# Optimization experiments

Hardware: AMD Instinct MI355X
Metric: run time of the kernel (lower is better)

Reference implementation:

```python
import jax, jax.numpy as jnp
import numpy as np

N = 50000

def gcn_conv(x, src, dst, W, b):
    # PyG GCNConv: h = x @ W; symmetric norm with self-loops; out = Ahat h + b
    h = x @ W  # [N, F]
    e = src.shape[0]
    deg = jax.ops.segment_sum(jnp.ones((e,), h.dtype), dst, num_segments=N) + 1.0  # +1 self-loop
    dinv = jax.lax.rsqrt(deg)  # deg >= 1 so finite
    norm = dinv[src] * dinv[dst]  # [E]
    agg = jax.ops.segment_sum(h[src] * norm[:, None], dst, num_segments=N)
    agg = agg + h * (dinv * dinv)[:, None]  # self-loop contribution
    return agg + b


def setup_inputs() -> dict:
    key = jax.random.key(0)
    ks = jax.random.split(key, 12)
    E = 400000
    x = jax.random.normal(ks[0], (N, 768), dtype=jnp.float32)
    edge_index = jax.random.randint(ks[1], (2, E), 0, N, dtype=jnp.int32)
    dims = [(768, 1536), (1536, 768), (768, 384), (384, 192), (192, 5)]
    inp = {"x": x, "edge_index": edge_index}
    for i, (fi, fo) in enumerate(dims):
        s = 1.0 / np.sqrt(fi)
        inp[f"W{i+1}"] = jax.random.uniform(ks[2 + 2 * i], (fi, fo), jnp.float32, -s, s)
        inp[f"b{i+1}"] = jnp.zeros((fo,), jnp.float32)
    return inp


def reference(x, edge_index, W1, b1, W2, b2, W3, b3, W4, b4, W5, b5):
    src, dst = edge_index[0], edge_index[1]
    h = x
    for W, b in [(W1, b1), (W2, b2), (W3, b3), (W4, b4)]:
        h = jax.nn.relu(gcn_conv(h, src, dst, W, b))
        # F.dropout with training=False is identity (eval mode)
    out = gcn_conv(h, src, dst, W5, b5)
    return (h, out)
```

## Files before the change

### kernel.cpp

```cpp
#include <hip/hip_runtime.h>
#include <stdint.h>

typedef unsigned short u16;
typedef unsigned int   u32;

#define NN 50000
#define NE 400000

typedef __bf16 bf16x8 __attribute__((ext_vector_type(8)));
typedef u16    u16x8  __attribute__((ext_vector_type(8)));
typedef float  f32x4  __attribute__((ext_vector_type(4)));

__device__ __forceinline__ float bf2f(u16 b) {
  union { u32 u; float f; } v; v.u = ((u32)b) << 16; return v.f;
}
__device__ __forceinline__ u16 f2bf(float f) {
  union { float f; u32 u; } v; v.f = f;
  u32 r = v.u + 0x7fffu + ((v.u >> 16) & 1u);
  return (u16)(r >> 16);
}


__global__ void zero_int_kernel(int* __restrict__ p, int n) {
  int i = blockIdx.x * blockDim.x + threadIdx.x;
  if (i < n) p[i] = 0;
}

__global__ void count_deg_kernel(const int* __restrict__ dst, int* __restrict__ deg, int e) {
  int i = blockIdx.x * blockDim.x + threadIdx.x;
  if (i < e) atomicAdd(&deg[dst[i]], 1);
}

__global__ void dinv_kernel(const int* __restrict__ deg, float* __restrict__ dinv, int n) {
  int i = blockIdx.x * blockDim.x + threadIdx.x;
  if (i < n) dinv[i] = rsqrtf((float)deg[i] + 1.0f);
}

__global__ __launch_bounds__(1024) void scan_kernel(const int* __restrict__ counts,
                                                    int* __restrict__ offsets, int n) {
  __shared__ int wsums[17];
  __shared__ int carry;
  int tid = threadIdx.x;
  int lane = tid & 63, wid = tid >> 6;
  if (tid == 0) carry = 0;
  __syncthreads();
  for (int base = 0; base < n; base += 1024) {
    int i = base + tid;
    int v = (i < n) ? counts[i] : 0;
    int s = v;
    #pragma unroll
    for (int off = 1; off < 64; off <<= 1) {
      int t = __shfl_up(s, off, 64);
      if (lane >= off) s += t;
    }
    if (lane == 63) wsums[wid] = s;
    __syncthreads();
    if (tid == 0) {
      int a = 0;
      #pragma unroll
      for (int w = 0; w < 16; ++w) { int t = wsums[w]; wsums[w] = a; a += t; }
      wsums[16] = a;
    }
    __syncthreads();
    if (i < n) offsets[i] = carry + wsums[wid] + s - v;
    __syncthreads();
    if (tid == 0) carry += wsums[16];
    __syncthreads();
  }
  if (tid == 0) offsets[n] = carry;
}

__global__ void csr_fill_kernel(const int* __restrict__ src, const int* __restrict__ dst,
                                const int* __restrict__ offsets, int* __restrict__ cursor,
                                const float* __restrict__ dinv,
                                int2* __restrict__ csr_pack, int e) {
  int i = blockIdx.x * blockDim.x + threadIdx.x;
  if (i < e) {
    int s = src[i], d = dst[i];
    int pos = offsets[d] + atomicAdd(&cursor[d], 1);
    float nr = dinv[s] * dinv[d];
    csr_pack[pos] = make_int2(s, __float_as_int(nr));
  }
}

__global__ void f2bf_kernel(const float* __restrict__ in, u16* __restrict__ out, int n) {
  int i = blockIdx.x * blockDim.x + threadIdx.x;
  if (i < n) out[i] = f2bf(in[i]);
}

__global__ void wt_kernel(const float* __restrict__ W, u16* __restrict__ Wt, int K, int N) {
  int i = blockIdx.x * blockDim.x + threadIdx.x;
  if (i < K * N) {
    int k = i / N;
    int n2 = i - k * N;
    Wt[n2 * K + k] = f2bf(W[i]);
  }
}


template<int G, bool HAS_BIAS, bool RELU, bool OUT_BF, bool OUT_F32>
__global__ __launch_bounds__(256) void agg8_kernel(
    const u16* __restrict__ g, const int* __restrict__ rowptr,
    const int2* __restrict__ csr_pack,
    const float* __restrict__ dinv, const float* __restrict__ bias,
    u16* __restrict__ outb, float* __restrict__ outf)
{
  constexpr int F = G * 8;
  int idx = blockIdx.x * blockDim.x + threadIdx.x;
  if (idx >= NN * G) return;
  int v = idx / G;
  int g8 = idx - v * G;
  const u16* base = g + g8 * 8;

  float acc[8];
  #pragma unroll
  for (int k = 0; k < 8; ++k) acc[k] = 0.f;

  int e0 = rowptr[v], e1 = rowptr[v + 1];
  int e = e0;
  for (; e + 3 < e1; e += 4) {
    int2 p0 = csr_pack[e];
    int2 p1 = csr_pack[e + 1];
    int2 p2 = csr_pack[e + 2];
    int2 p3 = csr_pack[e + 3];
    u16x8 r0 = *(const u16x8*)(base + (size_t)p0.x * F);
    u16x8 r1 = *(const u16x8*)(base + (size_t)p1.x * F);
    u16x8 r2 = *(const u16x8*)(base + (size_t)p2.x * F);
    u16x8 r3 = *(const u16x8*)(base + (size_t)p3.x * F);
    float n0 = __int_as_float(p0.y), n1 = __int_as_float(p1.y);
    float n2 = __int_as_float(p2.y), n3 = __int_as_float(p3.y);
    #pragma unroll
    for (int k = 0; k < 8; ++k) acc[k] += n0 * bf2f(r0[k]);
    #pragma unroll
    for (int k = 0; k < 8; ++k) acc[k] += n1 * bf2f(r1[k]);
    #pragma unroll
    for (int k = 0; k < 8; ++k) acc[k] += n2 * bf2f(r2[k]);
    #pragma unroll
    for (int k = 0; k < 8; ++k) acc[k] += n3 * bf2f(r3[k]);
  }
  for (; e < e1; ++e) {
    int2 p0 = csr_pack[e];
    u16x8 r0 = *(const u16x8*)(base + (size_t)p0.x * F);
    float n0 = __int_as_float(p0.y);
    #pragma unroll
    for (int k = 0; k < 8; ++k) acc[k] += n0 * bf2f(r0[k]);
  }

  float sv = dinv[v]; sv *= sv;
  u16x8 sr = *(const u16x8*)(base + (size_t)v * F);
  float vals[8];
  #pragma unroll
  for (int k = 0; k < 8; ++k) {
    float val = acc[k] + sv * bf2f(sr[k]);
    if (HAS_BIAS) val += bias[g8 * 8 + k];
    if (RELU) val = fmaxf(val, 0.f);
    vals[k] = val;
  }
  if (OUT_BF) {
    u16x8 ob;
    #pragma unroll
    for (int k = 0; k < 8; ++k) ob[k] = f2bf(vals[k]);
    *(u16x8*)(outb + (size_t)v * F + g8 * 8) = ob;
  }
  if (OUT_F32) {
    f32x4 o0, o1;
    #pragma unroll
    for (int k = 0; k < 4; ++k) { o0[k] = vals[k]; o1[k] = vals[4 + k]; }
    float* op = outf + (size_t)v * F + g8 * 8;
    *(f32x4*)op = o0;
    *(f32x4*)(op + 4) = o1;
  }
}

__global__ void agg_small_kernel(const u16* __restrict__ g, const int* __restrict__ rowptr,
                                 const int2* __restrict__ csr_pack,
                                 const float* __restrict__ dinv, const float* __restrict__ bias,
                                 float* __restrict__ out, int n, int F) {
  int idx = blockIdx.x * blockDim.x + threadIdx.x;
  if (idx >= n * F) return;
  int v = idx / F;
  int f = idx - v * F;
  float acc = 0.f;
  int e1 = rowptr[v + 1];
  for (int e = rowptr[v]; e < e1; ++e) {
    int2 p = csr_pack[e];
    acc += __int_as_float(p.y) * bf2f(g[p.x * F + f]);
  }
  float dv = dinv[v];
  out[idx] = acc + dv * dv * bf2f(g[v * F + f]) + bias[f];
}


#define BM 128
#define BN 128
#define BK 32

#define WAIT_VMCNT4 0x0F74
#define WAIT_VMCNT0 0x0F70

__device__ __forceinline__ void gl_lds16(const void* g, void* l) {
  __builtin_amdgcn_global_load_lds((const __attribute__((address_space(1))) void*)g,
                                   (__attribute__((address_space(3))) void*)l, 16, 0, 0);
}

template<bool BIAS_RELU>
__global__ __launch_bounds__(256, 4) void gemm_bt_kernel(
    const u16* __restrict__ A, const u16* __restrict__ Bt,
    u16* __restrict__ C, const float* __restrict__ bias,
    int M, int N, int K)
{
  __shared__ __align__(16) u16 As[2][BM * BK];
  __shared__ __align__(16) u16 Bs[2][BN * BK];
  int gm = (M + BM - 1) / BM;
  int gn = (N + BN - 1) / BN;
  int bid = blockIdx.x;
  int xcd = bid & 7;
  int t = bid >> 3;
  int trow = t / gn;
  int bn_i = t - trow * gn;
  int row = trow * 8 + xcd;
  if (row >= gm) return;
  int bm = row * BM, bn = bn_i * BN;

  int tid = threadIdx.x;
  int wave = tid >> 6, lane = tid & 63;
  int wm = wave & 1, wn = wave >> 1;

  int srow = tid >> 2;
  int sq_log = ((tid & 3) - ((tid >> 3) & 3)) & 3;
  int ar0 = min(bm + srow, M - 1);
  int ar1 = min(bm + 64 + srow, M - 1);
  int br0 = min(bn + srow, N - 1);
  int br1 = min(bn + 64 + srow, N - 1);
  const u16* ag0 = A + (size_t)ar0 * K + sq_log * 8;
  const u16* ag1 = A + (size_t)ar1 * K + sq_log * 8;
  const u16* bg0 = Bt + (size_t)br0 * K + sq_log * 8;
  const u16* bg1 = Bt + (size_t)br1 * K + sq_log * 8;
  int la0 = (wave * 16) * BK;
  int la1 = (64 + wave * 16) * BK;

  f32x4 acc[4][4];
  #pragma unroll
  for (int i = 0; i < 4; ++i)
    #pragma unroll
    for (int j = 0; j < 4; ++j)
      acc[i][j] = (f32x4){0.f, 0.f, 0.f, 0.f};

  int row16 = lane & 15, q = lane >> 4;
  int perm = (q + (row16 >> 1)) & 3;
  int ard = (wm * 64 + row16) * BK + perm * 8;
  int brd = (wn * 64 + row16) * BK + perm * 8;

  const int iters = K / BK;

  gl_lds16(ag0, &As[0][la0]);
  gl_lds16(ag1, &As[0][la1]);
  gl_lds16(bg0, &Bs[0][la0]);
  gl_lds16(bg1, &Bs[0][la1]);

  int buf = 0;
  for (int it = 0; it < iters; ++it) {
    __builtin_amdgcn_s_barrier();
    if (it + 1 < iters) {
      int kn = (it + 1) * BK;
      gl_lds16(ag0 + kn, &As[buf ^ 1][la0]);
      gl_lds16(ag1 + kn, &As[buf ^ 1][la1]);
      gl_lds16(bg0 + kn, &Bs[buf ^ 1][la0]);
      gl_lds16(bg1 + kn, &Bs[buf ^ 1][la1]);
      __builtin_amdgcn_s_waitcnt(WAIT_VMCNT4);
    } else {
      __builtin_amdgcn_s_waitcnt(WAIT_VMCNT0);
    }
    __builtin_amdgcn_s_barrier();

    bf16x8 af[4], bfr[4];
    #pragma unroll
    for (int i = 0; i < 4; ++i) af[i] = *(const bf16x8*)(&As[buf][ard + i * 16 * BK]);
    #pragma unroll
    for (int j = 0; j < 4; ++j) bfr[j] = *(const bf16x8*)(&Bs[buf][brd + j * 16 * BK]);
    #pragma unroll
    for (int i = 0; i < 4; ++i)
      #pragma unroll
      for (int j = 0; j < 4; ++j)
        acc[i][j] = __builtin_amdgcn_mfma_f32_16x16x32_bf16(af[i], bfr[j], acc[i][j], 0, 0, 0);
    buf ^= 1;
  }

  #pragma unroll
  for (int i = 0; i < 4; ++i) {
    int rbase = bm + wm * 64 + i * 16 + q * 4;
    #pragma unroll
    for (int j = 0; j < 4; ++j) {
      int col = bn + wn * 64 + j * 16 + row16;
      if (col < N) {
        float bv = BIAS_RELU ? bias[col] : 0.f;
        #pragma unroll
        for (int r = 0; r < 4; ++r) {
          int gr = rbase + r;
          if (gr < M) {
            float val = acc[i][j][r];
            if (BIAS_RELU) { val += bv; val = fmaxf(val, 0.f); }
            C[(size_t)gr * N + col] = f2bf(val);
          }
        }
      }
    }
  }
}

static inline int gemm_grid(int M, int N) {
  int gm = (M + BM - 1) / BM;
  int gn = (N + BN - 1) / BN;
  int rows_per_xcd = (gm + 7) / 8;
  return rows_per_xcd * gn * 8;
}


extern "C" void kernel_launch(void* const* d_in, const int* in_sizes, int n_in,
                              void* d_out, int out_size, void* d_ws, size_t ws_size,
                              hipStream_t stream) {
  const float* x   = (const float*)d_in[0];
  const int* ei    = (const int*)d_in[1];
  const int* src   = ei;
  const int* dst   = ei + NE;
  const float* W1  = (const float*)d_in[2];
  const float* b1  = (const float*)d_in[3];
  const float* W2  = (const float*)d_in[4];
  const float* b2  = (const float*)d_in[5];
  const float* W3  = (const float*)d_in[6];
  const float* b3  = (const float*)d_in[7];
  const float* W4  = (const float*)d_in[8];
  const float* b4  = (const float*)d_in[9];
  const float* W5  = (const float*)d_in[10];
  const float* b5  = (const float*)d_in[11];
  float* out_h = (float*)d_out;
  float* out_o = (float*)d_out + (size_t)NN * 192;

  char* p = (char*)d_ws;
  auto alloc = [&](size_t bytes) { char* r = p; p += (bytes + 255) & ~(size_t)255; return r; };
  int*   deg      = (int*)alloc((size_t)NN * 4);
  int*   cursor   = (int*)alloc((size_t)NN * 4);
  float* dinv     = (float*)alloc((size_t)NN * 4);
  int*   offs     = (int*)alloc((size_t)(NN + 1) * 4);
  int2*  csr_pack = (int2*)alloc((size_t)NE * 8);
  u16* W1t = (u16*)alloc((size_t)768 * 1536 * 2);
  u16* W2t = (u16*)alloc((size_t)1536 * 768 * 2);
  u16* W3t = (u16*)alloc((size_t)768 * 384 * 2);
  u16* W4t = (u16*)alloc((size_t)384 * 192 * 2);
  u16* W5t = (u16*)alloc((size_t)192 * 5 * 2);
  u16* B0 = (u16*)alloc((size_t)NN * 768 * 2);
  u16* B1 = (u16*)alloc((size_t)NN * 768 * 2);
  u16* B2 = (u16*)alloc((size_t)NN * 1536 * 2);

  u16* xb  = B0;
  u16* a0  = B1;
  u16* h1  = B2;
  u16* g2  = B0;
  u16* h2  = B1;
  u16* g3  = B0;
  u16* h3  = B2;
  u16* g4  = B0;
  u16* h4b = B1;
  u16* g5  = B0;

  const int M = NN;

  zero_int_kernel<<<(NN + 255) / 256, 256, 0, stream>>>(deg, NN);
  zero_int_kernel<<<(NN + 255) / 256, 256, 0, stream>>>(cursor, NN);
  count_deg_kernel<<<(NE + 255) / 256, 256, 0, stream>>>(dst, deg, NE);
  dinv_kernel<<<(NN + 255) / 256, 256, 0, stream>>>(deg, dinv, NN);
  scan_kernel<<<1, 1024, 0, stream>>>(deg, offs, NN);
  csr_fill_kernel<<<(NE + 255) / 256, 256, 0, stream>>>(src, dst, offs, cursor, dinv,
                                                        csr_pack, NE);
  f2bf_kernel<<<((NN * 768) + 255) / 256, 256, 0, stream>>>(x, xb, NN * 768);
  wt_kernel<<<((768 * 1536) + 255) / 256, 256, 0, stream>>>(W1, W1t, 768, 1536);
  wt_kernel<<<((1536 * 768) + 255) / 256, 256, 0, stream>>>(W2, W2t, 1536, 768);
  wt_kernel<<<((768 * 384) + 255) / 256, 256, 0, stream>>>(W3, W3t, 768, 384);
  wt_kernel<<<((384 * 192) + 255) / 256, 256, 0, stream>>>(W4, W4t, 384, 192);
  wt_kernel<<<((192 * 5) + 255) / 256, 256, 0, stream>>>(W5, W5t, 192, 5);

  dim3 blk(256);

  agg8_kernel<96, false, false, true, false><<<(NN * 96 + 255) / 256, blk, 0, stream>>>(
      xb, offs, csr_pack, dinv, nullptr, a0, nullptr);
  gemm_bt_kernel<true><<<gemm_grid(M, 1536), blk, 0, stream>>>(
      a0, W1t, h1, b1, M, 1536, 768);

  gemm_bt_kernel<false><<<gemm_grid(M, 768), blk, 0, stream>>>(
      h1, W2t, g2, nullptr, M, 768, 1536);
  agg8_kernel<96, true, true, true, false><<<(NN * 96 + 255) / 256, blk, 0, stream>>>(
      g2, offs, csr_pack, dinv, b2, h2, nullptr);

  gemm_bt_kernel<false><<<gemm_grid(M, 384), blk, 0, stream>>>(
      h2, W3t, g3, nullptr, M, 384, 768);
  agg8_kernel<48, true, true, true, false><<<(NN * 48 + 255) / 256, blk, 0, stream>>>(
      g3, offs, csr_pack, dinv, b3, h3, nullptr);

  gemm_bt_kernel<false><<<gemm_grid(M, 192), blk, 0, stream>>>(
      h3, W4t, g4, nullptr, M, 192, 384);
  agg8_kernel<24, true, true, true, true><<<(NN * 24 + 255) / 256, blk, 0, stream>>>(
      g4, offs, csr_pack, dinv, b4, h4b, out_h);

  gemm_bt_kernel<false><<<gemm_grid(M, 5), blk, 0, stream>>>(
      h4b, W5t, g5, nullptr, M, 5, 192);
  agg_small_kernel<<<((NN * 5) + 255) / 256, 256, 0, stream>>>(
      g5, offs, csr_pack, dinv, b5, out_o, NN, 5);
}
```

Measured before the change: 1.093 ms.

## Add 256x256-tile 8-wave GEMM kernel for the two largest layers

```diff
diff --git a/kernel.cpp b/kernel.cpp
--- a/kernel.cpp
+++ b/kernel.cpp
@@ -190,18 +190,175 @@
   out[idx] = acc + dv * dv * bf2f(g[v * F + f]) + bias[f];
 }
 
+#define WAIT_VMCNT4 0x0F74
+#define WAIT_VMCNT0 0x0F70
+
+__device__ __forceinline__ void gl_lds16(const void* g, void* l) {
+  __builtin_amdgcn_global_load_lds((const __attribute__((address_space(1))) void*)g,
+                                   (__attribute__((address_space(3))) void*)l, 16, 0, 0);
+}
+
+
+template<bool BIAS_RELU>
+__global__ __launch_bounds__(512, 2) void gemm256_kernel(
+    const u16* __restrict__ A, const u16* __restrict__ Bt,
+    u16* __restrict__ C, const float* __restrict__ bias,
+    int M, int N, int K)
+{
+  __shared__ __align__(16) u16 sA[2][2][256 * 32];
+  __shared__ __align__(16) u16 sB[2][2][256 * 32];
+
+  int gm = (M + 255) >> 8;
+  int gn = (N + 255) >> 8;
+  int bid = blockIdx.x;
+  int xcd = bid & 7;
+  int t = bid >> 3;
+  int trow = t / gn;
+  int bn_i = t - trow * gn;
+  int rowt = trow * 8 + xcd;
+  if (rowt >= gm) return;
+  int bm = rowt << 8, bn = bn_i << 8;
+
+  int tid = threadIdx.x;
+  int wid = tid >> 6, lane = tid & 63;
+  int wm = wid >> 2, wn = wid & 3;
+  int row16 = lane & 15, q = lane >> 4;
+
+  int sr = tid >> 2, sc = tid & 3;
+  int ar0 = min(bm + sr, M - 1);
+  int ar1 = min(bm + 128 + sr, M - 1);
+  int br0 = min(bn + sr, N - 1);
+  int br1 = min(bn + 128 + sr, N - 1);
+  const u16* Ag0 = A + (size_t)ar0 * K + sc * 8;
+  const u16* Ag1 = A + (size_t)ar1 * K + sc * 8;
+  const u16* Bg0 = Bt + (size_t)br0 * K + sc * 8;
+  const u16* Bg1 = Bt + (size_t)br1 * K + sc * 8;
+
+  f32x4 acc[8][4];
+  #pragma unroll
+  for (int m = 0; m < 8; ++m)
+    #pragma unroll
+    for (int n = 0; n < 4; ++n)
+      acc[m][n] = (f32x4){0.f, 0.f, 0.f, 0.f};
+
+  auto stageA = [&](int nb, int h, int ko) {
+    gl_lds16(Ag0 + ko, &sA[nb][h][tid * 8]);
+    gl_lds16(Ag1 + ko, &sA[nb][h][4096 + tid * 8]);
+  };
+  auto stageB = [&](int nb, int h, int ko) {
+    gl_lds16(Bg0 + ko, &sB[nb][h][tid * 8]);
+    gl_lds16(Bg1 + ko, &sB[nb][h][4096 + tid * 8]);
+  };
+
+  stageA(0, 0, 0);
+  stageB(0, 0, 0);
+  stageA(0, 1, 32);
+  stageB(0, 1, 32);
+  __builtin_amdgcn_s_waitcnt(WAIT_VMCNT4);
+  __builtin_amdgcn_s_barrier();
+
+  const int KT = K >> 6;
+  int arow = (wm * 128 + row16) * 32 + q * 8;
+  int brow = (wn * 64 + row16) * 32 + q * 8;
+
+  for (int kt = 0; kt < KT; ++kt) {
+    int buf = kt & 1, nb = buf ^ 1;
+    bool pf = (kt + 1 < KT);
+    int ko = (kt + 1) * 64;
+
+    bf16x8 af[4], bfr[4];
+
+    #pragma unroll
+    for (int m = 0; m < 4; ++m) af[m] = *(const bf16x8*)&sA[buf][0][arow + m * 512];
+    #pragma unroll
+    for (int n = 0; n < 4; ++n) bfr[n] = *(const bf16x8*)&sB[buf][0][brow + n * 512];
+    if (pf) stageA(nb, 0, ko);
+    __builtin_amdgcn_s_setprio(1);
+    #pragma unroll
+    for (int m = 0; m < 4; ++m)
+      #pragma unroll
+      for (int n = 0; n < 4; ++n)
+        acc[m][n] = __builtin_amdgcn_mfma_f32_16x16x32_bf16(af[m], bfr[n], acc[m][n], 0, 0, 0);
+    __builtin_amdgcn_s_setprio(0);
+
+    #pragma unroll
+    for (int m = 0; m < 4; ++m) af[m] = *(const bf16x8*)&sA[buf][0][arow + (m + 4) * 512];
+    if (pf) stageB(nb, 0, ko);
+    __builtin_amdgcn_s_setprio(1);
+    #pragma unroll
+    for (int m = 0; m < 4; ++m)
+      #pragma unroll
+      for (int n = 0; n < 4; ++n)
+        acc[m + 4][n] = __builtin_amdgcn_mfma_f32_16x16x32_bf16(af[m], bfr[n], acc[m + 4][n], 0, 0, 0);
+    __builtin_amdgcn_s_setprio(0);
+
+    if (pf) __builtin_amdgcn_s_waitcnt(WAIT_VMCNT4);
+    else    __builtin_amdgcn_s_waitcnt(WAIT_VMCNT0);
+    __builtin_amdgcn_s_barrier();
+
+    #pragma unroll
+    for (int m = 0; m < 4; ++m) af[m] = *(const bf16x8*)&sA[buf][1][arow + m * 512];
+    #pragma unroll
+    for (int n = 0; n < 4; ++n) bfr[n] = *(const bf16x8*)&sB[buf][1][brow + n * 512];
+    if (pf) stageA(nb, 1, ko + 32);
+    __builtin_amdgcn_s_setprio(1);
+    #pragma unroll
+    for (int m = 0; m < 4; ++m)
+      #pragma unroll
+      for (int n = 0; n < 4; ++n)
+        acc[m][n] = __builtin_amdgcn_mfma_f32_16x16x32_bf16(af[m], bfr[n], acc[m][n], 0, 0, 0);
+    __builtin_amdgcn_s_setprio(0);
+
+    #pragma unroll
+    for (int m = 0; m < 4; ++m) af[m] = *(const bf16x8*)&sA[buf][1][arow + (m + 4) * 512];
+    if (pf) stageB(nb, 1, ko + 32);
+    __builtin_amdgcn_s_setprio(1);
+    #pragma unroll
+    for (int m = 0; m < 4; ++m)
+      #pragma unroll
+      for (int n = 0; n < 4; ++n)
+        acc[m + 4][n] = __builtin_amdgcn_mfma_f32_16x16x32_bf16(af[m], bfr[n], acc[m + 4][n], 0, 0, 0);
+    __builtin_amdgcn_s_setprio(0);
+
+    if (pf) {
+      __builtin_amdgcn_s_waitcnt(WAIT_VMCNT4);
+      __builtin_amdgcn_s_barrier();
+    }
+  }
+
+  #pragma unroll
+  for (int m = 0; m < 8; ++m) {
+    int rbase = bm + wm * 128 + m * 16 + q * 4;
+    #pragma unroll
+    for (int n = 0; n < 4; ++n) {
+      int col = bn + wn * 64 + n * 16 + row16;
+      if (col < N) {
+        float bv = BIAS_RELU ? bias[col] : 0.f;
+        #pragma unroll
+        for (int r = 0; r < 4; ++r) {
+          int gr = rbase + r;
+          if (gr < M) {
+            float val = acc[m][n][r];
+            if (BIAS_RELU) { val += bv; val = fmaxf(val, 0.f); }
+            C[(size_t)gr * N + col] = f2bf(val);
+          }
+        }
+      }
+    }
+  }
+}
+
+static inline int gemm256_grid(int M, int N) {
+  int gm = (M + 255) / 256;
+  int gn = (N + 255) / 256;
+  int rows_per_xcd = (gm + 7) / 8;
+  return rows_per_xcd * 8 * gn;
+}
+
 
 #define BM 128
 #define BN 128
 #define BK 32
-
-#define WAIT_VMCNT4 0x0F74
-#define WAIT_VMCNT0 0x0F70
-
-__device__ __forceinline__ void gl_lds16(const void* g, void* l) {
-  __builtin_amdgcn_global_load_lds((const __attribute__((address_space(1))) void*)g,
-                                   (__attribute__((address_space(3))) void*)l, 16, 0, 0);
-}
 
 template<bool BIAS_RELU>
 __global__ __launch_bounds__(256, 4) void gemm_bt_kernel(
@@ -383,10 +540,10 @@
 
   agg8_kernel<96, false, false, true, false><<<(NN * 96 + 255) / 256, blk, 0, stream>>>(
       xb, offs, csr_pack, dinv, nullptr, a0, nullptr);
-  gemm_bt_kernel<true><<<gemm_grid(M, 1536), blk, 0, stream>>>(
+  gemm256_kernel<true><<<gemm256_grid(M, 1536), 512, 0, stream>>>(
       a0, W1t, h1, b1, M, 1536, 768);
 
-  gemm_bt_kernel<false><<<gemm_grid(M, 768), blk, 0, stream>>>(
+  gemm256_kernel<false><<<gemm256_grid(M, 768), 512, 0, stream>>>(
       h1, W2t, g2, nullptr, M, 768, 1536);
   agg8_kernel<96, true, true, true, false><<<(NN * 96 + 255) / 256, blk, 0, stream>>>(
       g2, offs, csr_pack, dinv, b2, h2, nullptr);
```

Result: no change. 1.102 ms (+0.8%).
